# Kernel tuning notes

Measured on AMD Instinct MI355X. Metric: run time of the kernel, lower is better.

The kernel has to match this reference:

```python
import jax, jax.numpy as jnp
import numpy as np

EMBED_DIM = 32
DELTA_V = 0.5
DELTA_D = 3.0
NUM_LABELS = 20  # instance labels are 1..NUM_LABELS; 0 is background


def _safe_sqrt(x):
    # sqrt with zero-safe gradient (matches norm of identical points -> 0)
    s = jnp.where(x > 0, x, 1.0)
    return jnp.where(x > 0, jnp.sqrt(s), 0.0)


def _per_batch(emb, seg):
    # emb: [D, N], seg: [N] int labels in 0..L (0 = background)
    D, N = emb.shape
    L = NUM_LABELS
    dt = emb.dtype
    ones = jnp.ones((N,), dt)
    counts = jax.ops.segment_sum(ones, seg, num_segments=L + 1)          # [L+1]
    sums = jax.ops.segment_sum(emb.T, seg, num_segments=L + 1)          # [L+1, D]
    means = sums / jnp.maximum(counts, 1.0)[:, None]                     # [L+1, D]
    present = (counts > 0).at[0].set(False)                              # [L+1]
    num_lanes = jnp.sum(present.astype(dt))

    # --- variance (pull) loss: each pixel vs its own instance centroid ---
    mpix = means[seg]                                                    # [N, D] gather
    sq = jnp.sum((emb.T - mpix) ** 2, axis=1)                            # [N]
    d = _safe_sqrt(sq)
    v = jnp.maximum(d - DELTA_V, 0.0) ** 2 * (seg > 0).astype(dt)        # background excluded
    vsum = jax.ops.segment_sum(v, seg, num_segments=L + 1)               # [L+1]
    vmean = vsum / jnp.maximum(counts, 1.0)
    var_loss = jnp.sum(vmean * present.astype(dt)) / jnp.maximum(num_lanes, 1.0)
    var_loss = jnp.where(num_lanes > 0, var_loss, jnp.zeros((), dt))

    # --- distance (push) loss between present centroids ---
    m = means[1:]                                                        # [L, D]
    p = present[1:]                                                      # [L]
    sqd = jnp.sum((m[:, None, :] - m[None, :, :]) ** 2, axis=-1)         # [L, L]
    dist = _safe_sqrt(sqd)
    pair = (p[:, None] & p[None, :]) & ~jnp.eye(L, dtype=bool)
    dl = jnp.sum(jnp.maximum(DELTA_D - dist, 0.0) ** 2 * pair.astype(dt))
    denom = jnp.maximum(num_lanes * (num_lanes - 1.0), 1.0)
    dist_loss = jnp.where(num_lanes > 1, dl / denom / 2.0, jnp.zeros((), dt))
    return var_loss, dist_loss


def setup_inputs() -> dict:
    key = jax.random.key(0)
    k1, k2 = jax.random.split(key)
    B, D, N = 8, EMBED_DIM, 65536  # 256x256 BEV raster flattened
    embedding = jax.random.normal(k1, (B, D, N), dtype=jnp.float32)
    seg_gt = jax.random.randint(k2, (B, N), 0, NUM_LABELS + 1, dtype=jnp.int32)
    return {"embedding": embedding, "seg_gt": seg_gt}


def reference(embedding, seg_gt):
    var_b, dist_b = jax.vmap(_per_batch)(embedding, seg_gt)  # [B], [B]
    var_loss = jnp.mean(var_b)
    dist_loss = jnp.mean(dist_b)
    reg_loss = jnp.zeros((), embedding.dtype)
    return (var_loss, dist_loss, reg_loss)
```

## Files before the change

### kernel.cpp

```cpp
#include <hip/hip_runtime.h>
#include <hip/hip_cooperative_groups.h>
namespace cg = cooperative_groups;

#define NSEG 21
#define NLBL 20
#define DIM  32
#define NS   64
#define NREP 16
#define DV   0.5f
#define DD   3.0f
#define BATCH 8
#define N_PIX 65536
#define SMS  36
#define DYNB (128*512 + 1024)

using short8 = __attribute__((ext_vector_type(8))) short;
using f32x4  = __attribute__((ext_vector_type(4))) float;

#define P_OFF  0
#define C2_OFF (BATCH*DIM*NLBL*NS)
#define V_OFF  (C2_OFF + BATCH*NLBL*NS)
#define PB_OFF (V_OFF + BATCH*NLBL*NS)

__device__ __forceinline__ short bf16rne(float f) {
  const unsigned u = __builtin_bit_cast(unsigned, f);
  return (short)((u + 0x7FFFu + ((u >> 16) & 1u)) >> 16);
}

__device__ __forceinline__ void momentsBody(const float* __restrict__ emb,
                                            const int* __restrict__ seg,
                                            float* __restrict__ ws,
                                            float* lred, ushort* tile,
                                            unsigned char* segt,
                                            int bx, int b, int tid) {
  const int wv = tid >> 6, lane = tid & 63;
  const int lr = lane & 15, lg = lane >> 4;
  const float* rowA0 = emb + ((size_t)b * DIM + lr) * N_PIX;
  const float* rowA1 = rowA0 + (size_t)16 * N_PIX;
  const int*   segb  = seg + (size_t)b * N_PIX;

  f32x4 s00 = {0,0,0,0}, s01 = {0,0,0,0}, s10 = {0,0,0,0}, s11 = {0,0,0,0};
  f32x4 c0  = {0,0,0,0}, c1  = {0,0,0,0};
  short8 ones;
  #pragma unroll
  for (int j = 0; j < 8; ++j) ones[j] = (short)0x3F80;

  #pragma unroll 2
  for (int t = 0; t < 8; ++t) {
    const int kl = wv * 256 + t * 32 + lg * 8;
    const int koff = bx * 1024 + kl;
    const float4 a00 = *(const float4*)(rowA0 + koff);
    const float4 a01 = *(const float4*)(rowA0 + koff + 4);
    const float4 a10 = *(const float4*)(rowA1 + koff);
    const float4 a11 = *(const float4*)(rowA1 + koff + 4);
    const int4   g0  = *(const int4*)(segb + koff);
    const int4   g1  = *(const int4*)(segb + koff + 4);

    short8 fa0, fa1, fb0, fb1;
    fa0[0] = bf16rne(a00.x); fa0[1] = bf16rne(a00.y);
    fa0[2] = bf16rne(a00.z); fa0[3] = bf16rne(a00.w);
    fa0[4] = bf16rne(a01.x); fa0[5] = bf16rne(a01.y);
    fa0[6] = bf16rne(a01.z); fa0[7] = bf16rne(a01.w);
    fa1[0] = bf16rne(a10.x); fa1[1] = bf16rne(a10.y);
    fa1[2] = bf16rne(a10.z); fa1[3] = bf16rne(a10.w);
    fa1[4] = bf16rne(a11.x); fa1[5] = bf16rne(a11.y);
    fa1[6] = bf16rne(a11.z); fa1[7] = bf16rne(a11.w);
    const int lab0 = lr + 1, lab1 = lr + 17;
    fb0[0] = (g0.x == lab0) ? (short)0x3F80 : (short)0;
    fb0[1] = (g0.y == lab0) ? (short)0x3F80 : (short)0;
    fb0[2] = (g0.z == lab0) ? (short)0x3F80 : (short)0;
    fb0[3] = (g0.w == lab0) ? (short)0x3F80 : (short)0;
    fb0[4] = (g1.x == lab0) ? (short)0x3F80 : (short)0;
    fb0[5] = (g1.y == lab0) ? (short)0x3F80 : (short)0;
    fb0[6] = (g1.z == lab0) ? (short)0x3F80 : (short)0;
    fb0[7] = (g1.w == lab0) ? (short)0x3F80 : (short)0;
    fb1[0] = (g0.x == lab1) ? (short)0x3F80 : (short)0;
    fb1[1] = (g0.y == lab1) ? (short)0x3F80 : (short)0;
    fb1[2] = (g0.z == lab1) ? (short)0x3F80 : (short)0;
    fb1[3] = (g0.w == lab1) ? (short)0x3F80 : (short)0;
    fb1[4] = (g1.x == lab1) ? (short)0x3F80 : (short)0;
    fb1[5] = (g1.y == lab1) ? (short)0x3F80 : (short)0;
    fb1[6] = (g1.z == lab1) ? (short)0x3F80 : (short)0;
    fb1[7] = (g1.w == lab1) ? (short)0x3F80 : (short)0;

    const int o = kl >> 3, om = o & 7;
    *(short8*)&tile[o * 256 + ((lr ^ om) << 3)] = fa0;
    *(short8*)&tile[o * 256 + (((lr ^ om) + 16) << 3)] = fa1;
    if (lr == 0) {
      unsigned long long pk =
          (unsigned long long)(g0.x & 255)        | ((unsigned long long)(g0.y & 255) << 8) |
          ((unsigned long long)(g0.z & 255) << 16) | ((unsigned long long)(g0.w & 255) << 24) |
          ((unsigned long long)(g1.x & 255) << 32) | ((unsigned long long)(g1.y & 255) << 40) |
          ((unsigned long long)(g1.z & 255) << 48) | ((unsigned long long)(g1.w & 255) << 56);
      *(unsigned long long*)&segt[o * 8] = pk;
    }

    s00 = __builtin_amdgcn_mfma_f32_16x16x32_bf16(fa0, fb0, s00, 0, 0, 0);
    s01 = __builtin_amdgcn_mfma_f32_16x16x32_bf16(fa0, fb1, s01, 0, 0, 0);
    s10 = __builtin_amdgcn_mfma_f32_16x16x32_bf16(fa1, fb0, s10, 0, 0, 0);
    s11 = __builtin_amdgcn_mfma_f32_16x16x32_bf16(fa1, fb1, s11, 0, 0, 0);
    c0  = __builtin_amdgcn_mfma_f32_16x16x32_bf16(ones, fb0, c0, 0, 0, 0);
    c1  = __builtin_amdgcn_mfma_f32_16x16x32_bf16(ones, fb1, c1, 0, 0, 0);
  }

  float vals[24];
  #pragma unroll
  for (int r = 0; r < 4; ++r) {
    vals[0 * 4 + r] = s00[r]; vals[1 * 4 + r] = s01[r];
    vals[2 * 4 + r] = s10[r]; vals[3 * 4 + r] = s11[r];
    vals[4 * 4 + r] = c0[r];  vals[5 * 4 + r] = c1[r];
  }
  #pragma unroll
  for (int w = 0; w < 4; ++w) {
    if (wv == w) {
      float* base = lred + lane * 4;
      if (w == 0) {
        #pragma unroll
        for (int f = 0; f < 6; ++f)
          #pragma unroll
          for (int r = 0; r < 4; ++r) base[f * 256 + r] = vals[f * 4 + r];
      } else {
        #pragma unroll
        for (int f = 0; f < 6; ++f)
          #pragma unroll
          for (int r = 0; r < 4; ++r) base[f * 256 + r] += vals[f * 4 + r];
      }
    }
    __syncthreads();
  }
  for (int i = tid; i < 1536; i += 256) {
    const float v = lred[i];
    const int f = i >> 8, ln = (i >> 2) & 63, r = i & 3;
    const int col = ln & 15, row = ((ln >> 4) << 2) | r;
    if (f < 4) {
      const int d = (f >> 1) * 16 + row;
      const int lcol = (f & 1) * 16 + col;
      if (lcol < NLBL)
        ws[P_OFF + (((size_t)(b * DIM + d) * NLBL) + lcol) * NS + bx] = v;
    } else {
      const int lcol = (f & 1) * 16 + col;
      if (row == 0 && lcol < NLBL)
        ws[C2_OFF + ((size_t)b * NLBL + lcol) * NS + bx] = v;
    }
  }
}

__device__ __forceinline__ void meansLocal(const float* __restrict__ ws,
                                           float* s_m, float* s_c, int* s_p,
                                           int b, int tid) {
  if (tid < 160) {
    const int g = tid >> 3, j = tid & 7;
    const float4* cp = (const float4*)(ws + C2_OFF + ((size_t)b * NLBL + g) * NS + j * 8);
    const float4 a = cp[0], c4 = cp[1];
    float c = a.x + a.y + a.z + a.w + c4.x + c4.y + c4.z + c4.w;
    c += __shfl_xor(c, 1, 64); c += __shfl_xor(c, 2, 64); c += __shfl_xor(c, 4, 64);
    if (j == 0) { s_c[g] = c; s_p[g] = (c > 0.f) ? 1 : 0; }
  }
  for (int i = tid; i < SMS; i += 256) s_m[i] = 0.f;
  __syncthreads();
  for (int i = tid; i < NLBL * DIM; i += 256) {
    const int d = i / NLBL, l = i - (i / NLBL) * NLBL;
    const float4* pp = (const float4*)(ws + P_OFF + ((size_t)b * DIM * NLBL + i) * NS);
    float q0 = 0.f, q1 = 0.f, q2 = 0.f, q3 = 0.f;
    #pragma unroll
    for (int k = 0; k < 16; k += 4) {
      const float4 v0 = pp[k], v1 = pp[k + 1], v2 = pp[k + 2], v3 = pp[k + 3];
      q0 += v0.x + v0.y + v0.z + v0.w;
      q1 += v1.x + v1.y + v1.z + v1.w;
      q2 += v2.x + v2.y + v2.z + v2.w;
      q3 += v3.x + v3.y + v3.z + v3.w;
    }
    s_m[(l + 1) * SMS + d] = (q0 + q1 + q2 + q3) / fmaxf(s_c[l], 1.f);
  }
}

__device__ __forceinline__ void varTile(const ushort* tile, const unsigned char* segt,
                                        const float* s_m, float* s_v,
                                        float* __restrict__ ws, int bx, int b, int tid) {
  const int px0 = tid * 4;
  const int o = px0 >> 3, om = o & 7, p8 = px0 & 7;
  const int la0 = segt[px0], la1 = segt[px0 + 1], la2 = segt[px0 + 2], la3 = segt[px0 + 3];
  float q0 = 0.f, q1 = 0.f, q2 = 0.f, q3 = 0.f;
  #pragma unroll
  for (int db = 0; db < 8; ++db) {
    const f32x4 m0 = *(const f32x4*)&s_m[la0 * SMS + db * 4];
    const f32x4 m1 = *(const f32x4*)&s_m[la1 * SMS + db * 4];
    const f32x4 m2 = *(const f32x4*)&s_m[la2 * SMS + db * 4];
    const f32x4 m3 = *(const f32x4*)&s_m[la3 * SMS + db * 4];
    #pragma unroll
    for (int dd = 0; dd < 4; ++dd) {
      const int d = db * 4 + dd;
      const ushort4 ev = *(const ushort4*)&tile[o * 256 + ((d ^ om) << 3) + p8];
      float t;
      t = __builtin_bit_cast(float, (unsigned)ev.x << 16) - m0[dd]; q0 += t * t;
      t = __builtin_bit_cast(float, (unsigned)ev.y << 16) - m1[dd]; q1 += t * t;
      t = __builtin_bit_cast(float, (unsigned)ev.z << 16) - m2[dd]; q2 += t * t;
      t = __builtin_bit_cast(float, (unsigned)ev.w << 16) - m3[dd]; q3 += t * t;
    }
  }
  const int rb = (tid & (NREP - 1)) * NSEG;
  if (la0 > 0) { const float r = sqrtf(q0) - DV; if (r > 0.f) atomicAdd(&s_v[rb + la0], r * r); }
  if (la1 > 0) { const float r = sqrtf(q1) - DV; if (r > 0.f) atomicAdd(&s_v[rb + la1], r * r); }
  if (la2 > 0) { const float r = sqrtf(q2) - DV; if (r > 0.f) atomicAdd(&s_v[rb + la2], r * r); }
  if (la3 > 0) { const float r = sqrtf(q3) - DV; if (r > 0.f) atomicAdd(&s_v[rb + la3], r * r); }
  __syncthreads();
  if (tid < NLBL) {
    float v = 0.f;
    #pragma unroll
    for (int r = 0; r < NREP; ++r) v += s_v[r * NSEG + (tid + 1)];
    ws[V_OFF + ((size_t)b * NLBL + tid) * NS + bx] = v;
  }
}

__device__ __forceinline__ void finalCore(const float* __restrict__ ws,
                                          const float* s_m, const float* s_c,
                                          const int* s_p, float* s_vs, float* s_red,
                                          int b, int tid, float* vb, float* db_) {
  const int wv = tid >> 6, lane = tid & 63;
  if (tid < 160) {
    const int g = tid >> 3, j = tid & 7;
    const float4* v4 = (const float4*)(ws + V_OFF + ((size_t)b * NLBL + g) * NS + j * 8);
    const float4 a = v4[0], c = v4[1];
    float s = a.x + a.y + a.z + a.w + c.x + c.y + c.z + c.w;
    s += __shfl_xor(s, 1, 64); s += __shfl_xor(s, 2, 64); s += __shfl_xor(s, 4, 64);
    if (j == 0) s_vs[g] = s;
  }
  __syncthreads();
  float dl = 0.f;
  for (int p = tid; p < NLBL * NLBL; p += 256) {
    const int i = p / NLBL, j = p - (p / NLBL) * NLBL;
    if (i != j && s_p[i] && s_p[j]) {
      float sq = 0.f;
      #pragma unroll
      for (int d = 0; d < DIM; ++d) {
        const float t = s_m[(i + 1) * SMS + d] - s_m[(j + 1) * SMS + d];
        sq += t * t;
      }
      const float r = DD - sqrtf(sq);
      if (r > 0.f) dl += r * r;
    }
  }
  #pragma unroll
  for (int off = 32; off; off >>= 1) dl += __shfl_xor(dl, off, 64);
  if (lane == 0) s_red[wv] = dl;
  __syncthreads();
  if (tid == 0) {
    const float dsum = s_red[0] + s_red[1] + s_red[2] + s_red[3];
    float nl = 0.f, var = 0.f;
    for (int l = 0; l < NLBL; ++l)
      if (s_p[l]) { nl += 1.f; var += s_vs[l] / s_c[l]; }
    *vb  = (nl > 0.f) ? var / nl : 0.f;
    *db_ = (nl > 1.f) ? dsum / fmaxf(nl * (nl - 1.f), 1.f) * 0.5f : 0.f;
  }
}

__global__ __launch_bounds__(256, 2)
void k_fused(const float* __restrict__ emb, const int* __restrict__ seg,
             float* __restrict__ ws, float* __restrict__ out) {
  extern __shared__ __align__(16) char dynls[];
  ushort* tile = (ushort*)dynls;
  unsigned char* segt = (unsigned char*)(dynls + 65536);
  __shared__ __align__(16) float lred[1536];
  __shared__ __align__(16) float s_m[NSEG * SMS];
  __shared__ float s_v[NREP * NSEG];
  __shared__ float s_c[NLBL];
  __shared__ float s_vs[NLBL];
  __shared__ int   s_p[NLBL];
  __shared__ float s_red[4];
  cg::grid_group gg = cg::this_grid();
  const int tid = threadIdx.x, bx = blockIdx.x, b = blockIdx.y;

  momentsBody(emb, seg, ws, lred, tile, segt, bx, b, tid);
  if (bx == 0 && b == 0 && tid < 3) out[tid] = 0.f;
  gg.sync();

  for (int i = tid; i < NREP * NSEG; i += 256) s_v[i] = 0.f;
  meansLocal(ws, s_m, s_c, s_p, b, tid);
  __syncthreads();
  varTile(tile, segt, s_m, s_v, ws, bx, b, tid);
  gg.sync();

  if (bx == 0) {
    float vb, db_;
    finalCore(ws, s_m, s_c, s_p, s_vs, s_red, b, tid, &vb, &db_);
    if (tid == 0) {
      atomicAdd(&out[0], vb * (1.f / BATCH));
      atomicAdd(&out[1], db_ * (1.f / BATCH));
    }
  }
}

__global__ __launch_bounds__(256)
void k_moments(const float* __restrict__ emb, const int* __restrict__ seg,
               float* __restrict__ ws) {
  extern __shared__ __align__(16) char dynls[];
  ushort* tile = (ushort*)dynls;
  unsigned char* segt = (unsigned char*)(dynls + 65536);
  __shared__ __align__(16) float lred[1536];
  momentsBody(emb, seg, ws, lred, tile, segt, blockIdx.x, blockIdx.y, threadIdx.x);
}
__global__ __launch_bounds__(256)
void k_varG(const float* __restrict__ emb, const int* __restrict__ seg,
            float* __restrict__ ws) {
  __shared__ __align__(16) float s_m[NSEG * SMS];
  __shared__ float s_v[NREP * NSEG];
  __shared__ float s_c[NLBL];
  __shared__ int   s_p[NLBL];
  const int tid = threadIdx.x, bx = blockIdx.x, b = blockIdx.y;
  for (int i = tid; i < NREP * NSEG; i += 256) s_v[i] = 0.f;
  meansLocal(ws, s_m, s_c, s_p, b, tid);
  __syncthreads();
  const int n0 = bx * 1024 + tid * 4;
  const int4 sl = *(const int4*)(seg + (size_t)b * N_PIX + n0);
  const float4* e4 = (const float4*)(emb + (size_t)b * DIM * N_PIX + n0);
  float q0 = 0.f, q1 = 0.f, q2 = 0.f, q3 = 0.f;
  #pragma unroll 8
  for (int d = 0; d < DIM; ++d) {
    const float4 e = e4[d * (N_PIX / 4)];
    float t;
    t = e.x - s_m[sl.x * SMS + d]; q0 += t * t;
    t = e.y - s_m[sl.y * SMS + d]; q1 += t * t;
    t = e.z - s_m[sl.z * SMS + d]; q2 += t * t;
    t = e.w - s_m[sl.w * SMS + d]; q3 += t * t;
  }
  const int rb = (tid & (NREP - 1)) * NSEG;
  if (sl.x > 0) { const float r = sqrtf(q0) - DV; if (r > 0.f) atomicAdd(&s_v[rb + sl.x], r * r); }
  if (sl.y > 0) { const float r = sqrtf(q1) - DV; if (r > 0.f) atomicAdd(&s_v[rb + sl.y], r * r); }
  if (sl.z > 0) { const float r = sqrtf(q2) - DV; if (r > 0.f) atomicAdd(&s_v[rb + sl.z], r * r); }
  if (sl.w > 0) { const float r = sqrtf(q3) - DV; if (r > 0.f) atomicAdd(&s_v[rb + sl.w], r * r); }
  __syncthreads();
  if (tid < NLBL) {
    float v = 0.f;
    #pragma unroll
    for (int r = 0; r < NREP; ++r) v += s_v[r * NSEG + (tid + 1)];
    ws[V_OFF + ((size_t)b * NLBL + tid) * NS + bx] = v;
  }
}
__global__ __launch_bounds__(256)
void k_final(float* __restrict__ ws) {
  __shared__ __align__(16) float s_m[NSEG * SMS];
  __shared__ float s_c[NLBL];
  __shared__ float s_vs[NLBL];
  __shared__ int   s_p[NLBL];
  __shared__ float s_red[4];
  const int b = blockIdx.x, tid = threadIdx.x;
  meansLocal(ws, s_m, s_c, s_p, b, tid);
  __syncthreads();
  float vb, db_;
  finalCore(ws, s_m, s_c, s_p, s_vs, s_red, b, tid, &vb, &db_);
  if (tid == 0) {
    ws[PB_OFF + b * 2]     = vb;
    ws[PB_OFF + b * 2 + 1] = db_;
  }
}
__global__ __launch_bounds__(64)
void k_out(const float* __restrict__ ws, float* __restrict__ out) {
  const int tid = threadIdx.x;
  float v = 0.f, d = 0.f;
  if (tid < BATCH) {
    v = ws[PB_OFF + tid * 2];
    d = ws[PB_OFF + tid * 2 + 1];
  }
  #pragma unroll
  for (int off = 4; off; off >>= 1) { v += __shfl_xor(v, off, 64); d += __shfl_xor(d, off, 64); }
  if (tid == 0) {
    out[0] = v / (float)BATCH;
    out[1] = d / (float)BATCH;
    out[2] = 0.f;
  }
}

extern "C" void kernel_launch(void* const* d_in, const int* in_sizes, int n_in,
                              void* d_out, int out_size, void* d_ws, size_t ws_size,
                              hipStream_t stream) {
  const float* emb = (const float*)d_in[0];
  const int*   seg = (const int*)d_in[1];
  float* out = (float*)d_out;
  float* ws  = (float*)d_ws;

  int maxB = 0;
  bool coop = false;
  if (hipOccupancyMaxActiveBlocksPerMultiprocessor(&maxB, (const void*)k_fused, 256, DYNB)
        == hipSuccess)
    coop = ((long)maxB * 256 >= (long)NS * BATCH);
  if (coop) {
    void* args[] = {(void*)&emb, (void*)&seg, (void*)&ws, (void*)&out};
    if (hipLaunchCooperativeKernel((const void*)k_fused, dim3(NS, BATCH), dim3(256),
                                   args, DYNB, stream) == hipSuccess)
      return;
  }
  k_moments<<<dim3(NS, BATCH), 256, DYNB, stream>>>(emb, seg, ws);
  k_varG   <<<dim3(NS, BATCH), 256, 0, stream>>>(emb, seg, ws);
  k_final  <<<dim3(BATCH), 256, 0, stream>>>(ws);
  k_out    <<<1, 64, 0, stream>>>(ws, out);
}
```

Before: 51.17 us.

## Replace grid-wide syncs with per-batch atomic counters and last-block reductions

Swaps the two cooperative grid syncs for per-batch arrival counters. The last block to finish each batch computes the means once and publishes them through a flag that the other blocks spin on, and the last variance block does that batch's final reduction. Means are now computed once per batch and stored in the workspace instead of being recomputed by every block. The change adds a memset launch to reset the counters and relies on spin-waiting while all blocks are co-resident, still under a cooperative launch.

Result: slower. 52.44 us (+2.5%).

```diff
diff --git a/kernel.cpp b/kernel.cpp
--- a/kernel.cpp
+++ b/kernel.cpp
@@ -1,6 +1,5 @@
 #include <hip/hip_runtime.h>
 #include <hip/hip_cooperative_groups.h>
-namespace cg = cooperative_groups;
 
 #define NSEG 21
 #define NLBL 20
@@ -12,15 +11,20 @@
 #define BATCH 8
 #define N_PIX 65536
 #define SMS  36
-#define DYNB (128*512 + 1024)
+#define TILE_B 65536
+#define SEGT_B 1024
+#define DYNB  (TILE_B + SEGT_B)
 
 using short8 = __attribute__((ext_vector_type(8))) short;
 using f32x4  = __attribute__((ext_vector_type(4))) float;
 
 #define P_OFF  0
 #define C2_OFF (BATCH*DIM*NLBL*NS)
-#define V_OFF  (C2_OFF + BATCH*NLBL*NS)
+#define M_OFF  (C2_OFF + BATCH*NLBL*NS)
+#define CN_OFF (M_OFF + BATCH*NLBL*DIM)
+#define V_OFF  (CN_OFF + BATCH*NLBL)
 #define PB_OFF (V_OFF + BATCH*NLBL*NS)
+#define BAR_OFF (PB_OFF + 16)
 
 __device__ __forceinline__ short bf16rne(float f) {
   const unsigned u = __builtin_bit_cast(unsigned, f);
@@ -145,22 +149,23 @@
   }
 }
 
-__device__ __forceinline__ void meansLocal(const float* __restrict__ ws,
-                                           float* s_m, float* s_c, int* s_p,
-                                           int b, int tid) {
+__device__ __forceinline__ void meansSolo(float* __restrict__ ws, float* s_c,
+                                          int b, int tid) {
   if (tid < 160) {
     const int g = tid >> 3, j = tid & 7;
     const float4* cp = (const float4*)(ws + C2_OFF + ((size_t)b * NLBL + g) * NS + j * 8);
     const float4 a = cp[0], c4 = cp[1];
     float c = a.x + a.y + a.z + a.w + c4.x + c4.y + c4.z + c4.w;
     c += __shfl_xor(c, 1, 64); c += __shfl_xor(c, 2, 64); c += __shfl_xor(c, 4, 64);
-    if (j == 0) { s_c[g] = c; s_p[g] = (c > 0.f) ? 1 : 0; }
-  }
-  for (int i = tid; i < SMS; i += 256) s_m[i] = 0.f;
-  __syncthreads();
-  for (int i = tid; i < NLBL * DIM; i += 256) {
-    const int d = i / NLBL, l = i - (i / NLBL) * NLBL;
-    const float4* pp = (const float4*)(ws + P_OFF + ((size_t)b * DIM * NLBL + i) * NS);
+    if (j == 0) {
+      ws[CN_OFF + b * NLBL + g] = c;
+      s_c[g] = fmaxf(c, 1.f);
+    }
+  }
+  __syncthreads();
+  for (int m = tid; m < NLBL * DIM; m += 256) {
+    const int l = m >> 5, d = m & 31;
+    const float4* pp = (const float4*)(ws + P_OFF + (((size_t)(b * DIM + d) * NLBL) + l) * NS);
     float q0 = 0.f, q1 = 0.f, q2 = 0.f, q3 = 0.f;
     #pragma unroll
     for (int k = 0; k < 16; k += 4) {
@@ -170,7 +175,19 @@
       q2 += v2.x + v2.y + v2.z + v2.w;
       q3 += v3.x + v3.y + v3.z + v3.w;
     }
-    s_m[(l + 1) * SMS + d] = (q0 + q1 + q2 + q3) / fmaxf(s_c[l], 1.f);
+    ws[M_OFF + (size_t)b * NLBL * DIM + m] = (q0 + q1 + q2 + q3) / s_c[l];
+  }
+}
+
+__device__ __forceinline__ void loadMeans(const float* __restrict__ ws,
+                                          float* s_m, int b, int tid) {
+  for (int i = tid; i < NSEG * SMS; i += 256) s_m[i] = 0.f;
+  __syncthreads();
+  if (tid < 160) {
+    const float4 v = ((const float4*)(ws + M_OFF + (size_t)b * NLBL * DIM))[tid];
+    const int flat = tid * 4, l = flat >> 5, d = flat & 31;
+    float* dst = &s_m[(l + 1) * SMS + d];
+    dst[0] = v.x; dst[1] = v.y; dst[2] = v.z; dst[3] = v.w;
   }
 }
 
@@ -213,8 +230,8 @@
 }
 
 __device__ __forceinline__ void finalCore(const float* __restrict__ ws,
-                                          const float* s_m, const float* s_c,
-                                          const int* s_p, float* s_vs, float* s_red,
+                                          const float* s_m, float* s_c, float* s_vs,
+                                          int* s_p, float* s_red,
                                           int b, int tid, float* vb, float* db_) {
   const int wv = tid >> 6, lane = tid & 63;
   if (tid < 160) {
@@ -224,6 +241,11 @@
     float s = a.x + a.y + a.z + a.w + c.x + c.y + c.z + c.w;
     s += __shfl_xor(s, 1, 64); s += __shfl_xor(s, 2, 64); s += __shfl_xor(s, 4, 64);
     if (j == 0) s_vs[g] = s;
+  }
+  if (tid < NLBL) {
+    const float c = ws[CN_OFF + b * NLBL + tid];
+    s_c[tid] = c;
+    s_p[tid] = (c > 0.f) ? 1 : 0;
   }
   __syncthreads();
   float dl = 0.f;
@@ -259,7 +281,7 @@
              float* __restrict__ ws, float* __restrict__ out) {
   extern __shared__ __align__(16) char dynls[];
   ushort* tile = (ushort*)dynls;
-  unsigned char* segt = (unsigned char*)(dynls + 65536);
+  unsigned char* segt = (unsigned char*)(dynls + TILE_B);
   __shared__ __align__(16) float lred[1536];
   __shared__ __align__(16) float s_m[NSEG * SMS];
   __shared__ float s_v[NREP * NSEG];
@@ -267,25 +289,63 @@
   __shared__ float s_vs[NLBL];
   __shared__ int   s_p[NLBL];
   __shared__ float s_red[4];
-  cg::grid_group gg = cg::this_grid();
+  __shared__ int   s_last;
   const int tid = threadIdx.x, bx = blockIdx.x, b = blockIdx.y;
+  unsigned* bar  = (unsigned*)(ws + BAR_OFF);
+  unsigned* ctrA = bar;
+  unsigned* mRdy = bar + 8;
+  unsigned* ctrC = bar + 16;
+  unsigned* done = bar + 24;
 
   momentsBody(emb, seg, ws, lred, tile, segt, bx, b, tid);
-  if (bx == 0 && b == 0 && tid < 3) out[tid] = 0.f;
-  gg.sync();
+
+  if (tid == 0) {
+    __threadfence();
+    s_last = (atomicAdd(&ctrA[b], 1u) == NS - 1) ? 1 : 0;
+  }
+  __syncthreads();
+  if (s_last) {
+    __threadfence();
+    meansSolo(ws, s_c, b, tid);
+    __syncthreads();
+    if (tid == 0) { __threadfence(); atomicAdd(&mRdy[b], 1u); }
+  }
+  if (tid == 0) {
+    while (atomicAdd(&mRdy[b], 0u) == 0u) __builtin_amdgcn_s_sleep(2);
+    __threadfence();
+  }
+  __syncthreads();
 
   for (int i = tid; i < NREP * NSEG; i += 256) s_v[i] = 0.f;
-  meansLocal(ws, s_m, s_c, s_p, b, tid);
+  loadMeans(ws, s_m, b, tid);
   __syncthreads();
   varTile(tile, segt, s_m, s_v, ws, bx, b, tid);
-  gg.sync();
-
-  if (bx == 0) {
+
+  if (tid == 0) {
+    __threadfence();
+    s_last = (atomicAdd(&ctrC[b], 1u) == NS - 1) ? 1 : 0;
+  }
+  __syncthreads();
+  if (s_last) {
+    __threadfence();
     float vb, db_;
-    finalCore(ws, s_m, s_c, s_p, s_vs, s_red, b, tid, &vb, &db_);
+    finalCore(ws, s_m, s_c, s_vs, s_p, s_red, b, tid, &vb, &db_);
     if (tid == 0) {
-      atomicAdd(&out[0], vb * (1.f / BATCH));
-      atomicAdd(&out[1], db_ * (1.f / BATCH));
+      ws[PB_OFF + b * 2]     = vb;
+      ws[PB_OFF + b * 2 + 1] = db_;
+      __threadfence();
+      if (atomicAdd(done, 1u) == BATCH - 1) {
+        __threadfence();
+        float v = 0.f, dsum = 0.f;
+        #pragma unroll
+        for (int i = 0; i < BATCH; ++i) {
+          v    += atomicAdd(&ws[PB_OFF + i * 2], 0.f);
+          dsum += atomicAdd(&ws[PB_OFF + i * 2 + 1], 0.f);
+        }
+        out[0] = v / (float)BATCH;
+        out[1] = dsum / (float)BATCH;
+        out[2] = 0.f;
+      }
     }
   }
 }
@@ -295,20 +355,23 @@
                float* __restrict__ ws) {
   extern __shared__ __align__(16) char dynls[];
   ushort* tile = (ushort*)dynls;
-  unsigned char* segt = (unsigned char*)(dynls + 65536);
+  unsigned char* segt = (unsigned char*)(dynls + TILE_B);
   __shared__ __align__(16) float lred[1536];
   momentsBody(emb, seg, ws, lred, tile, segt, blockIdx.x, blockIdx.y, threadIdx.x);
+}
+__global__ __launch_bounds__(256)
+void k_means(float* __restrict__ ws) {
+  __shared__ float s_c[NLBL];
+  meansSolo(ws, s_c, blockIdx.x, threadIdx.x);
 }
 __global__ __launch_bounds__(256)
 void k_varG(const float* __restrict__ emb, const int* __restrict__ seg,
             float* __restrict__ ws) {
   __shared__ __align__(16) float s_m[NSEG * SMS];
   __shared__ float s_v[NREP * NSEG];
-  __shared__ float s_c[NLBL];
-  __shared__ int   s_p[NLBL];
   const int tid = threadIdx.x, bx = blockIdx.x, b = blockIdx.y;
   for (int i = tid; i < NREP * NSEG; i += 256) s_v[i] = 0.f;
-  meansLocal(ws, s_m, s_c, s_p, b, tid);
+  loadMeans(ws, s_m, b, tid);
   __syncthreads();
   const int n0 = bx * 1024 + tid * 4;
   const int4 sl = *(const int4*)(seg + (size_t)b * N_PIX + n0);
@@ -344,10 +407,10 @@
   __shared__ int   s_p[NLBL];
   __shared__ float s_red[4];
   const int b = blockIdx.x, tid = threadIdx.x;
-  meansLocal(ws, s_m, s_c, s_p, b, tid);
+  loadMeans(ws, s_m, b, tid);
   __syncthreads();
   float vb, db_;
-  finalCore(ws, s_m, s_c, s_p, s_vs, s_red, b, tid, &vb, &db_);
+  finalCore(ws, s_m, s_c, s_vs, s_p, s_red, b, tid, &vb, &db_);
   if (tid == 0) {
     ws[PB_OFF + b * 2]     = vb;
     ws[PB_OFF + b * 2 + 1] = db_;
@@ -377,6 +440,8 @@
   const int*   seg = (const int*)d_in[1];
   float* out = (float*)d_out;
   float* ws  = (float*)d_ws;
+
+  hipMemsetAsync(ws + BAR_OFF, 0, 32 * sizeof(unsigned), stream);
 
   int maxB = 0;
   bool coop = false;
@@ -390,6 +455,7 @@
       return;
   }
   k_moments<<<dim3(NS, BATCH), 256, DYNB, stream>>>(emb, seg, ws);
+  k_means  <<<dim3(BATCH), 256, 0, stream>>>(ws);
   k_varG   <<<dim3(NS, BATCH), 256, 0, stream>>>(emb, seg, ws);
   k_final  <<<dim3(BATCH), 256, 0, stream>>>(ws);
   k_out    <<<1, 64, 0, stream>>>(ws, out);
```
